# Optimization experiments

Hardware: AMD Instinct MI355X
Metric: run time of the kernel (lower is better)

The kernel has to match this reference:

```python
import jax, jax.numpy as jnp
import numpy as np

B, S, D, H = 2, 2048, 1024, 16
HD = D // H  # head_dim = 64

def setup_inputs() -> dict:
    key = jax.random.key(0)
    ks = jax.random.split(key, 6)
    scale = 1.0 / np.sqrt(D)  # ~xavier for square matrices
    return {
        "x": jax.random.normal(ks[0], (B, S, D), dtype=jnp.float32),
        "Wq": jax.random.normal(ks[1], (D, D), dtype=jnp.float32) * scale,
        "bq": jnp.zeros((D,), dtype=jnp.float32),
        "Wk": jax.random.normal(ks[2], (D, D), dtype=jnp.float32) * scale,
        "bk": jnp.zeros((D,), dtype=jnp.float32),
        "Wv": jax.random.normal(ks[3], (D, D), dtype=jnp.float32) * scale,
        "bv": jnp.zeros((D,), dtype=jnp.float32),
        "Wo": jax.random.normal(ks[4], (D, D), dtype=jnp.float32) * scale,
        "bo": jnp.zeros((D,), dtype=jnp.float32),
    }

def reference(x, Wq, bq, Wk, bk, Wv, bv, Wo, bo):
    b, s, d = x.shape
    # projections (torch Linear: x @ W^T + b)
    q = (x @ Wq.T + bq).reshape(b, s, H, HD).transpose(0, 2, 1, 3)  # [b,h,s,hd]
    k = (x @ Wk.T + bk).reshape(b, s, H, HD).transpose(0, 2, 1, 3)
    v = (x @ Wv.T + bv).reshape(b, s, H, HD).transpose(0, 2, 1, 3)
    scores = jnp.einsum('bhqd,bhkd->bhqk', q, k) / jnp.sqrt(jnp.float32(HD))
    attn = jax.nn.softmax(scores, axis=-1)  # dropout is identity in eval mode
    out = jnp.einsum('bhqk,bhkd->bhqd', attn, v)
    out = out.transpose(0, 2, 1, 3).reshape(b, s, d)
    return out @ Wo.T + bo
```

## Files before the change

kernel.cpp:

```cpp
#include <hip/hip_runtime.h>
#include <hip/hip_bf16.h>

constexpr int NH   = 16;
constexpr int SEQ  = 2048;
constexpr int DM   = 1024;
constexpr int HDIM = 64;

typedef __attribute__((ext_vector_type(4)))  float f32x4;
typedef __attribute__((ext_vector_type(16))) float f32x16;
typedef __attribute__((ext_vector_type(8)))  short bf16x8;

typedef __attribute__((address_space(3))) unsigned int lds_u32_t;
typedef const __attribute__((address_space(1))) unsigned int glb_u32_t;

__device__ __forceinline__ void gll16(const void* g, void* l) {
  __builtin_amdgcn_global_load_lds((glb_u32_t*)g, (lds_u32_t*)l, 16, 0, 0);
}

__device__ __forceinline__ ushort f2bf(float f) {
  union { float f; unsigned u; } v; v.f = f;
  unsigned u = v.u;
  return (ushort)((u + 0x7fffu + ((u >> 16) & 1u)) >> 16);
}

__device__ __forceinline__ float fast_exp2(float x) {
#if __has_builtin(__builtin_amdgcn_exp2f)
  return __builtin_amdgcn_exp2f(x);
#else
  return __expf(x * 0.69314718056f);
#endif
}

__device__ __forceinline__ unsigned cvtpk(float a, float b) {
  unsigned r;
  asm("v_cvt_pk_bf16_f32 %0, %1, %2" : "=v"(r) : "v"(a), "v"(b));
  return r;
}

__device__ __forceinline__ void plswap(unsigned &a, unsigned &b) {
  asm("v_permlane32_swap_b32 %0, %1" : "+v"(a), "+v"(b));
}

__global__ void cast_all(const float* __restrict__ x,
                         const float* __restrict__ wq, const float* __restrict__ wk,
                         const float* __restrict__ wv, const float* __restrict__ wo,
                         ushort* __restrict__ xb, ushort* __restrict__ wqkv,
                         ushort* __restrict__ wob) {
  const int i = blockIdx.x * blockDim.x + threadIdx.x;
  const float* src; ushort* dst; int off;
  if (i < 1048576)      { src = x;  dst = xb;             off = i; }
  else if (i < 1310720) { src = wq; dst = wqkv;           off = i - 1048576; }
  else if (i < 1572864) { src = wk; dst = wqkv + 1048576; off = i - 1310720; }
  else if (i < 1835008) { src = wv; dst = wqkv + 2097152; off = i - 1572864; }
  else                  { src = wo; dst = wob;            off = i - 1835008; }
  const float4 v = reinterpret_cast<const float4*>(src)[off];
  ushort4 o;
  o.x = f2bf(v.x); o.y = f2bf(v.y); o.z = f2bf(v.z); o.w = f2bf(v.w);
  reinterpret_cast<ushort4*>(dst)[off] = o;
}

__global__ __launch_bounds__(256) void gemm_qkv(
    const ushort* __restrict__ A, const ushort* __restrict__ Bw,
    const float* __restrict__ bq, const float* __restrict__ bk, const float* __restrict__ bv,
    ushort* __restrict__ qh, ushort* __restrict__ kh, ushort* __restrict__ vth)
{
  __shared__ ushort As[128 * 32];
  __shared__ ushort Bs[128 * 32];
  const int tid = threadIdx.x;
  const int lane = tid & 63, wid = tid >> 6;
  const int wr = wid >> 1, wc = wid & 1;
  const int l15 = lane & 15, lhi = lane >> 4;
  const int bm = blockIdx.x, bn = blockIdx.y;

  f32x4 acc[4][4] = {};

  const int strow = tid >> 2;
  const int stcol = (tid & 3) * 8;
  const ushort* Ag0 = A  + (size_t)(bm * 128 + strow) * 1024 + stcol;
  const ushort* Ag1 = Ag0 + 64 * 1024;
  const ushort* Bg0 = Bw + (size_t)(bn * 128 + strow) * 1024 + stcol;
  const ushort* Bg1 = Bg0 + 64 * 1024;
  ushort* Asl = As + tid * 8;
  ushort* Bsl = Bs + tid * 8;

  for (int k0 = 0; k0 < 1024; k0 += 32) {
    gll16(Ag0 + k0, Asl);
    gll16(Ag1 + k0, Asl + 2048);
    gll16(Bg0 + k0, Bsl);
    gll16(Bg1 + k0, Bsl + 2048);
    __syncthreads();
    bf16x8 af[4], bf[4];
#pragma unroll
    for (int i = 0; i < 4; i++)
      af[i] = *reinterpret_cast<const bf16x8*>(As + (wr * 64 + i * 16 + l15) * 32 + lhi * 8);
#pragma unroll
    for (int j = 0; j < 4; j++)
      bf[j] = *reinterpret_cast<const bf16x8*>(Bs + (wc * 64 + j * 16 + l15) * 32 + lhi * 8);
#pragma unroll
    for (int i = 0; i < 4; i++)
#pragma unroll
      for (int j = 0; j < 4; j++)
        acc[i][j] = __builtin_amdgcn_mfma_f32_16x16x32_bf16(af[i], bf[j], acc[i][j], 0, 0, 0);
    __syncthreads();
  }

  const int ncol0 = bn * 128 + wc * 64;
  const int mrow0 = bm * 128 + wr * 64;
  const int which = ncol0 >> 10;

  if (which == 2) {
#pragma unroll
    for (int i = 0; i < 4; i++) {
#pragma unroll
      for (int j = 0; j < 4; j++) {
        const int nn = (ncol0 + j * 16 + l15) & 1023;
        const int h = nn >> 6, hd = nn & 63;
        const float bias = bv[nn];
        const int m0 = mrow0 + i * 16 + lhi * 4;
        const int b = m0 >> 11, s = m0 & 2047;
        ushort4 pk;
        pk.x = f2bf(acc[i][j][0] + bias);
        pk.y = f2bf(acc[i][j][1] + bias);
        pk.z = f2bf(acc[i][j][2] + bias);
        pk.w = f2bf(acc[i][j][3] + bias);
        *reinterpret_cast<ushort4*>(
            &vth[((size_t)(b * NH + h) * HDIM + hd) * SEQ + s]) = pk;
      }
    }
  } else {
    const float scl = (which == 0) ? 0.18033688f : 1.0f;
    const float* __restrict__ bptr = (which == 0) ? bq : bk;
    ushort* __restrict__ dst = (which == 0) ? qh : kh;
#pragma unroll
    for (int i = 0; i < 4; i++) {
#pragma unroll
      for (int j = 0; j < 4; j++) {
        const int nn = (ncol0 + j * 16 + l15) & 1023;
        const int h = nn >> 6, hd = nn & 63;
        const float bias = bptr[nn];
#pragma unroll
        for (int jr = 0; jr < 4; jr++) {
          const int m = mrow0 + i * 16 + lhi * 4 + jr;
          const int b = m >> 11, s = m & 2047;
          dst[((size_t)(b * NH + h) * SEQ + s) * HDIM + hd] = f2bf((acc[i][j][jr] + bias) * scl);
        }
      }
    }
  }
}

__global__ __launch_bounds__(512, 2) void attn_kernel(
    const ushort* __restrict__ qh, const ushort* __restrict__ kh,
    const ushort* __restrict__ vth, ushort* __restrict__ ctx)
{
  __shared__ __align__(16) ushort Kt[2][64 * 64];
  __shared__ __align__(16) ushort Vt[2][64 * 64];
  __shared__ float linv_s[8][32];
  const int tid = threadIdx.x, lane = tid & 63, wid = tid >> 6;
  const int l31 = lane & 31, hi = lane >> 5;
  const int bh = blockIdx.y;
  const int q0 = blockIdx.x * 256;
  const int qw = q0 + wid * 32;
  const int rswz = (lane & 7) << 4;
  const int hi16 = hi * 16;

  bf16x8 qf[4];
  const ushort* qb = qh + (size_t)bh * SEQ * HDIM;
#pragma unroll
  for (int st = 0; st < 4; st++)
    qf[st] = *reinterpret_cast<const bf16x8*>(
        qb + (size_t)(qw + l31) * HDIM + st * 16 + hi * 8);

  f32x16 o0 = {}, o1 = {};
  float mrow = -INFINITY, lrow = 0.f;

  const int srow = tid >> 3;
  const int scole = (((tid & 7) * 16) ^ ((srow & 7) << 4)) >> 1;
  const ushort* kbase = kh + (size_t)bh * SEQ * HDIM;
  const ushort* vbase = vth + (size_t)bh * HDIM * SEQ;

  auto stage = [&](int buf, int kv0) {
    gll16(kbase + (size_t)(kv0 + srow) * HDIM + scole, &Kt[buf][tid * 8]);
    gll16(vbase + (size_t)srow * SEQ + kv0 + scole, &Vt[buf][tid * 8]);
  };

  stage(0, 0);
  __syncthreads();

  for (int t = 0; t < SEQ / 64; ++t) {
    const int cur = t & 1;
    if (t < SEQ / 64 - 1) stage(cur ^ 1, (t + 1) * 64);

    const char* kb = (const char*)Kt[cur];
    bf16x8 kf0[4], kf1[4];
#pragma unroll
    for (int st = 0; st < 4; st++) {
      kf0[st] = *reinterpret_cast<const bf16x8*>(kb + l31 * 128 + ((st * 32 + hi16) ^ rswz));
      kf1[st] = *reinterpret_cast<const bf16x8*>(kb + (32 + l31) * 128 + ((st * 32 + hi16) ^ rswz));
    }
    f32x16 acc0 = {}, acc1 = {};
    __builtin_amdgcn_s_setprio(1);
#pragma unroll
    for (int st = 0; st < 4; st++) {
      acc0 = __builtin_amdgcn_mfma_f32_32x32x16_bf16(kf0[st], qf[st], acc0, 0, 0, 0);
      acc1 = __builtin_amdgcn_mfma_f32_32x32x16_bf16(kf1[st], qf[st], acc1, 0, 0, 0);
    }
    __builtin_amdgcn_s_setprio(0);

    float tm[8];
#pragma unroll
    for (int r = 0; r < 8; r++)
      tm[r] = fmaxf(fmaxf(acc0[r], acc0[r + 8]), fmaxf(acc1[r], acc1[r + 8]));
    float mx = fmaxf(fmaxf(fmaxf(tm[0], tm[1]), fmaxf(tm[2], tm[3])),
                     fmaxf(fmaxf(tm[4], tm[5]), fmaxf(tm[6], tm[7])));
    mx = fmaxf(mx, __shfl_xor(mx, 32));
    if (__any(mx > mrow + 8.0f)) {
      const float mnew = fmaxf(mrow, mx);
      const float alpha = fast_exp2(mrow - mnew);
      mrow = mnew;
      lrow *= alpha;
      o0 *= alpha; o1 *= alpha;
    }
    float p0[16], p1[16];
#pragma unroll
    for (int r = 0; r < 16; r++) {
      p0[r] = fast_exp2(acc0[r] - mrow);
      p1[r] = fast_exp2(acc1[r] - mrow);
    }
    float ss[8];
#pragma unroll
    for (int r = 0; r < 8; r++) ss[r] = (p0[r] + p0[r + 8]) + (p1[r] + p1[r + 8]);
    float rs = ((ss[0] + ss[1]) + (ss[2] + ss[3])) + ((ss[4] + ss[5]) + (ss[6] + ss[7]));
    rs += __shfl_xor(rs, 32);
    lrow += rs;

    union PU { unsigned u[4]; bf16x8 v; };
    PU pa[4];
    {
      unsigned a0 = cvtpk(p0[0], p0[1]),   b0 = cvtpk(p0[4], p0[5]);   plswap(a0, b0);
      unsigned a1 = cvtpk(p0[2], p0[3]),   b1 = cvtpk(p0[6], p0[7]);   plswap(a1, b1);
      unsigned a2 = cvtpk(p0[8], p0[9]),   b2 = cvtpk(p0[12], p0[13]); plswap(a2, b2);
      unsigned a3 = cvtpk(p0[10], p0[11]), b3 = cvtpk(p0[14], p0[15]); plswap(a3, b3);
      pa[0].u[0] = a0; pa[0].u[1] = a1; pa[0].u[2] = b0; pa[0].u[3] = b1;
      pa[1].u[0] = a2; pa[1].u[1] = a3; pa[1].u[2] = b2; pa[1].u[3] = b3;
      unsigned c0 = cvtpk(p1[0], p1[1]),   d0 = cvtpk(p1[4], p1[5]);   plswap(c0, d0);
      unsigned c1 = cvtpk(p1[2], p1[3]),   d1 = cvtpk(p1[6], p1[7]);   plswap(c1, d1);
      unsigned c2 = cvtpk(p1[8], p1[9]),   d2 = cvtpk(p1[12], p1[13]); plswap(c2, d2);
      unsigned c3 = cvtpk(p1[10], p1[11]), d3 = cvtpk(p1[14], p1[15]); plswap(c3, d3);
      pa[2].u[0] = c0; pa[2].u[1] = c1; pa[2].u[2] = d0; pa[2].u[3] = d1;
      pa[3].u[0] = c2; pa[3].u[1] = c3; pa[3].u[2] = d2; pa[3].u[3] = d3;
    }

    const char* vb = (const char*)Vt[cur];
    bf16x8 bv0[4], bv1[4];
#pragma unroll
    for (int st = 0; st < 4; st++) {
      bv0[st] = *reinterpret_cast<const bf16x8*>(vb + l31 * 128 + ((st * 32 + hi16) ^ rswz));
      bv1[st] = *reinterpret_cast<const bf16x8*>(vb + (32 + l31) * 128 + ((st * 32 + hi16) ^ rswz));
    }
    __builtin_amdgcn_s_setprio(1);
#pragma unroll
    for (int st = 0; st < 4; st++) {
      o0 = __builtin_amdgcn_mfma_f32_32x32x16_bf16(pa[st].v, bv0[st], o0, 0, 0, 0);
      o1 = __builtin_amdgcn_mfma_f32_32x32x16_bf16(pa[st].v, bv1[st], o1, 0, 0, 0);
    }
    __builtin_amdgcn_s_setprio(0);

    __syncthreads();
  }

  const int b = bh >> 4, h = bh & 15;
  linv_s[wid][l31] = 1.0f / lrow;
  ushort* cb = ctx + (size_t)b * SEQ * DM + (size_t)h * HDIM;
#pragma unroll
  for (int r = 0; r < 16; r++) {
    const int qrow = (r & 3) + 8 * (r >> 2) + 4 * hi;
    const float iv = linv_s[wid][qrow];
    ushort* rp = cb + (size_t)(qw + qrow) * DM;
    rp[l31]      = f2bf(o0[r] * iv);
    rp[32 + l31] = f2bf(o1[r] * iv);
  }
}

__global__ __launch_bounds__(256) void gemm_out(
    const ushort* __restrict__ A, const ushort* __restrict__ Bw,
    const float* __restrict__ bo, float* __restrict__ out)
{
  __shared__ ushort As[128 * 32];
  __shared__ ushort Bs[128 * 32];
  const int tid = threadIdx.x;
  const int lane = tid & 63, wid = tid >> 6;
  const int wr = wid >> 1, wc = wid & 1;
  const int l15 = lane & 15, lhi = lane >> 4;
  const int bm = blockIdx.x, bn = blockIdx.y;

  f32x4 acc[4][4] = {};

  const int strow = tid >> 2;
  const int stcol = (tid & 3) * 8;
  const ushort* Ag0 = A  + (size_t)(bm * 128 + strow) * 1024 + stcol;
  const ushort* Ag1 = Ag0 + 64 * 1024;
  const ushort* Bg0 = Bw + (size_t)(bn * 128 + strow) * 1024 + stcol;
  const ushort* Bg1 = Bg0 + 64 * 1024;
  ushort* Asl = As + tid * 8;
  ushort* Bsl = Bs + tid * 8;

  for (int k0 = 0; k0 < 1024; k0 += 32) {
    gll16(Ag0 + k0, Asl);
    gll16(Ag1 + k0, Asl + 2048);
    gll16(Bg0 + k0, Bsl);
    gll16(Bg1 + k0, Bsl + 2048);
    __syncthreads();
    bf16x8 af[4], bf[4];
#pragma unroll
    for (int i = 0; i < 4; i++)
      af[i] = *reinterpret_cast<const bf16x8*>(As + (wr * 64 + i * 16 + l15) * 32 + lhi * 8);
#pragma unroll
    for (int j = 0; j < 4; j++)
      bf[j] = *reinterpret_cast<const bf16x8*>(Bs + (wc * 64 + j * 16 + l15) * 32 + lhi * 8);
#pragma unroll
    for (int i = 0; i < 4; i++)
#pragma unroll
      for (int j = 0; j < 4; j++)
        acc[i][j] = __builtin_amdgcn_mfma_f32_16x16x32_bf16(af[i], bf[j], acc[i][j], 0, 0, 0);
    __syncthreads();
  }

  const int ncol0 = bn * 128 + wc * 64;
  const int mrow0 = bm * 128 + wr * 64;
#pragma unroll
  for (int i = 0; i < 4; i++)
#pragma unroll
    for (int j = 0; j < 4; j++) {
      const int n = ncol0 + j * 16 + l15;
      const float bias = bo[n];
#pragma unroll
      for (int jr = 0; jr < 4; jr++) {
        const int m = mrow0 + i * 16 + lhi * 4 + jr;
        out[(size_t)m * 1024 + n] = acc[i][j][jr] + bias;
      }
    }
}

extern "C" void kernel_launch(void* const* d_in, const int* in_sizes, int n_in,
                              void* d_out, int out_size, void* d_ws, size_t ws_size,
                              hipStream_t stream) {
  (void)in_sizes; (void)n_in; (void)out_size; (void)ws_size;
  const float* x  = (const float*)d_in[0];
  const float* Wq = (const float*)d_in[1];
  const float* bq = (const float*)d_in[2];
  const float* Wk = (const float*)d_in[3];
  const float* bk = (const float*)d_in[4];
  const float* Wv = (const float*)d_in[5];
  const float* bv = (const float*)d_in[6];
  const float* Wo = (const float*)d_in[7];
  const float* bo = (const float*)d_in[8];
  float* out = (float*)d_out;

  char* ws = (char*)d_ws;
  ushort* xb   = (ushort*)(ws);
  ushort* wqkv = (ushort*)(ws + 8388608);
  ushort* wob  = (ushort*)(ws + 14680064);
  ushort* qhb  = (ushort*)(ws + 16777216);
  ushort* khb  = (ushort*)(ws + 25165824);
  ushort* vth  = (ushort*)(ws + 33554432);
  ushort* ctx  = (ushort*)(ws + 41943040);

  cast_all<<<8192, 256, 0, stream>>>(x, Wq, Wk, Wv, Wo, xb, wqkv, wob);
  gemm_qkv<<<dim3(32, 24), 256, 0, stream>>>(xb, wqkv, bq, bk, bv, qhb, khb, vth);
  attn_kernel<<<dim3(8, 32), 512, 0, stream>>>(qhb, khb, vth, ctx);
  gemm_out<<<dim3(32, 8), 256, 0, stream>>>(ctx, wob, bo, out);
}
```

Before: 214.4 us.

## Double-buffer GEMM tiles, enlarge attention KV tile to 128, remap attention grid

Both projection GEMMs now keep two LDS buffers and issue the global-to-LDS loads for the next K slice before computing the current one, with one barrier per step instead of two. The attention kernel now processes 128 keys per iteration instead of 64, with new swizzles for the wider V tile and K fragments loaded in chunks. It also uses a 1D grid where consecutive blocks walk the heads first. This halves the attention loop's barriers and per-tile softmax overhead, and aims to overlap GEMM loads with MFMA work, at the cost of doubled LDS use and higher register pressure in attention, which could reduce occupancy.

```diff
diff --git a/kernel.cpp b/kernel.cpp
--- a/kernel.cpp
+++ b/kernel.cpp
@@ -64,8 +64,8 @@
     const float* __restrict__ bq, const float* __restrict__ bk, const float* __restrict__ bv,
     ushort* __restrict__ qh, ushort* __restrict__ kh, ushort* __restrict__ vth)
 {
-  __shared__ ushort As[128 * 32];
-  __shared__ ushort Bs[128 * 32];
+  __shared__ ushort As[2][128 * 32];
+  __shared__ ushort Bs[2][128 * 32];
   const int tid = threadIdx.x;
   const int lane = tid & 63, wid = tid >> 6;
   const int wr = wid >> 1, wc = wid & 1;
@@ -80,22 +80,27 @@
   const ushort* Ag1 = Ag0 + 64 * 1024;
   const ushort* Bg0 = Bw + (size_t)(bn * 128 + strow) * 1024 + stcol;
   const ushort* Bg1 = Bg0 + 64 * 1024;
-  ushort* Asl = As + tid * 8;
-  ushort* Bsl = Bs + tid * 8;
-
-  for (int k0 = 0; k0 < 1024; k0 += 32) {
-    gll16(Ag0 + k0, Asl);
-    gll16(Ag1 + k0, Asl + 2048);
-    gll16(Bg0 + k0, Bsl);
-    gll16(Bg1 + k0, Bsl + 2048);
-    __syncthreads();
+
+  auto stage = [&](int buf, int k0) {
+    gll16(Ag0 + k0, &As[buf][tid * 8]);
+    gll16(Ag1 + k0, &As[buf][tid * 8 + 2048]);
+    gll16(Bg0 + k0, &Bs[buf][tid * 8]);
+    gll16(Bg1 + k0, &Bs[buf][tid * 8 + 2048]);
+  };
+
+  stage(0, 0);
+  __syncthreads();
+
+  for (int kk = 0; kk < 32; ++kk) {
+    const int cur = kk & 1;
+    if (kk < 31) stage(cur ^ 1, (kk + 1) * 32);
     bf16x8 af[4], bf[4];
 #pragma unroll
     for (int i = 0; i < 4; i++)
-      af[i] = *reinterpret_cast<const bf16x8*>(As + (wr * 64 + i * 16 + l15) * 32 + lhi * 8);
+      af[i] = *reinterpret_cast<const bf16x8*>(&As[cur][(wr * 64 + i * 16 + l15) * 32 + lhi * 8]);
 #pragma unroll
     for (int j = 0; j < 4; j++)
-      bf[j] = *reinterpret_cast<const bf16x8*>(Bs + (wc * 64 + j * 16 + l15) * 32 + lhi * 8);
+      bf[j] = *reinterpret_cast<const bf16x8*>(&Bs[cur][(wc * 64 + j * 16 + l15) * 32 + lhi * 8]);
 #pragma unroll
     for (int i = 0; i < 4; i++)
 #pragma unroll
@@ -153,15 +158,17 @@
     const ushort* __restrict__ qh, const ushort* __restrict__ kh,
     const ushort* __restrict__ vth, ushort* __restrict__ ctx)
 {
-  __shared__ __align__(16) ushort Kt[2][64 * 64];
-  __shared__ __align__(16) ushort Vt[2][64 * 64];
+  __shared__ __align__(16) ushort Kt[2][128 * 64];
+  __shared__ __align__(16) ushort Vt[2][64 * 128];
   __shared__ float linv_s[8][32];
   const int tid = threadIdx.x, lane = tid & 63, wid = tid >> 6;
   const int l31 = lane & 31, hi = lane >> 5;
-  const int bh = blockIdx.y;
-  const int q0 = blockIdx.x * 256;
+  const int bid = blockIdx.x;
+  const int bh = bid & 31;
+  const int q0 = (bid >> 5) * 256;
   const int qw = q0 + wid * 32;
-  const int rswz = (lane & 7) << 4;
+  const int kswz = (l31 & 7) << 4;
+  const int vswz = (l31 & 15) << 4;
   const int hi16 = hi * 16;
 
   bf16x8 qf[4];
@@ -174,45 +181,78 @@
   f32x16 o0 = {}, o1 = {};
   float mrow = -INFINITY, lrow = 0.f;
 
-  const int srow = tid >> 3;
-  const int scole = (((tid & 7) * 16) ^ ((srow & 7) << 4)) >> 1;
+  const int srK = tid >> 3;
+  const int scK = (((tid & 7) * 16) ^ ((srK & 7) << 4)) >> 1;
+  const int srV = tid >> 4;
+  const int scV = (((tid & 15) * 16) ^ ((srV & 15) << 4)) >> 1;
   const ushort* kbase = kh + (size_t)bh * SEQ * HDIM;
   const ushort* vbase = vth + (size_t)bh * HDIM * SEQ;
 
   auto stage = [&](int buf, int kv0) {
-    gll16(kbase + (size_t)(kv0 + srow) * HDIM + scole, &Kt[buf][tid * 8]);
-    gll16(vbase + (size_t)srow * SEQ + kv0 + scole, &Vt[buf][tid * 8]);
+    gll16(kbase + (size_t)(kv0 + srK) * HDIM + scK,      &Kt[buf][tid * 8]);
+    gll16(kbase + (size_t)(kv0 + 64 + srK) * HDIM + scK, &Kt[buf][tid * 8 + 4096]);
+    gll16(vbase + (size_t)srV * SEQ + kv0 + scV,         &Vt[buf][tid * 8]);
+    gll16(vbase + (size_t)(32 + srV) * SEQ + kv0 + scV,  &Vt[buf][tid * 8 + 4096]);
   };
 
   stage(0, 0);
   __syncthreads();
 
-  for (int t = 0; t < SEQ / 64; ++t) {
+  union PU { unsigned u[4]; bf16x8 v; };
+  auto mkpa = [&](const f32x16& p, PU& lo, PU& hi_) {
+    unsigned a0 = cvtpk(p[0], p[1]),   b0 = cvtpk(p[4], p[5]);   plswap(a0, b0);
+    unsigned a1 = cvtpk(p[2], p[3]),   b1 = cvtpk(p[6], p[7]);   plswap(a1, b1);
+    unsigned a2 = cvtpk(p[8], p[9]),   b2 = cvtpk(p[12], p[13]); plswap(a2, b2);
+    unsigned a3 = cvtpk(p[10], p[11]), b3 = cvtpk(p[14], p[15]); plswap(a3, b3);
+    lo.u[0] = a0;  lo.u[1] = a1;  lo.u[2] = b0;  lo.u[3] = b1;
+    hi_.u[0] = a2; hi_.u[1] = a3; hi_.u[2] = b2; hi_.u[3] = b3;
+  };
+
+  for (int t = 0; t < SEQ / 128; ++t) {
     const int cur = t & 1;
-    if (t < SEQ / 64 - 1) stage(cur ^ 1, (t + 1) * 64);
+    if (t < SEQ / 128 - 1) stage(cur ^ 1, (t + 1) * 128);
 
     const char* kb = (const char*)Kt[cur];
-    bf16x8 kf0[4], kf1[4];
-#pragma unroll
-    for (int st = 0; st < 4; st++) {
-      kf0[st] = *reinterpret_cast<const bf16x8*>(kb + l31 * 128 + ((st * 32 + hi16) ^ rswz));
-      kf1[st] = *reinterpret_cast<const bf16x8*>(kb + (32 + l31) * 128 + ((st * 32 + hi16) ^ rswz));
-    }
-    f32x16 acc0 = {}, acc1 = {};
+    f32x16 acc0 = {}, acc1 = {}, acc2 = {}, acc3 = {};
     __builtin_amdgcn_s_setprio(1);
-#pragma unroll
-    for (int st = 0; st < 4; st++) {
-      acc0 = __builtin_amdgcn_mfma_f32_32x32x16_bf16(kf0[st], qf[st], acc0, 0, 0, 0);
-      acc1 = __builtin_amdgcn_mfma_f32_32x32x16_bf16(kf1[st], qf[st], acc1, 0, 0, 0);
+    {
+      bf16x8 kf[4];
+#pragma unroll
+      for (int st = 0; st < 4; st++)
+        kf[st] = *reinterpret_cast<const bf16x8*>(kb + l31 * 128 + ((st * 32 + hi16) ^ kswz));
+#pragma unroll
+      for (int st = 0; st < 4; st++)
+        acc0 = __builtin_amdgcn_mfma_f32_32x32x16_bf16(kf[st], qf[st], acc0, 0, 0, 0);
+#pragma unroll
+      for (int st = 0; st < 4; st++)
+        kf[st] = *reinterpret_cast<const bf16x8*>(kb + (32 + l31) * 128 + ((st * 32 + hi16) ^ kswz));
+#pragma unroll
+      for (int st = 0; st < 4; st++)
+        acc1 = __builtin_amdgcn_mfma_f32_32x32x16_bf16(kf[st], qf[st], acc1, 0, 0, 0);
+#pragma unroll
+      for (int st = 0; st < 4; st++)
+        kf[st] = *reinterpret_cast<const bf16x8*>(kb + (64 + l31) * 128 + ((st * 32 + hi16) ^ kswz));
+#pragma unroll
+      for (int st = 0; st < 4; st++)
+        acc2 = __builtin_amdgcn_mfma_f32_32x32x16_bf16(kf[st], qf[st], acc2, 0, 0, 0);
+#pragma unroll
+      for (int st = 0; st < 4; st++)
+        kf[st] = *reinterpret_cast<const bf16x8*>(kb + (96 + l31) * 128 + ((st * 32 + hi16) ^ kswz));
+#pragma unroll
+      for (int st = 0; st < 4; st++)
+        acc3 = __builtin_amdgcn_mfma_f32_32x32x16_bf16(kf[st], qf[st], acc3, 0, 0, 0);
     }
     __builtin_amdgcn_s_setprio(0);
 
-    float tm[8];
-#pragma unroll
-    for (int r = 0; r < 8; r++)
-      tm[r] = fmaxf(fmaxf(acc0[r], acc0[r + 8]), fmaxf(acc1[r], acc1[r + 8]));
-    float mx = fmaxf(fmaxf(fmaxf(tm[0], tm[1]), fmaxf(tm[2], tm[3])),
-                     fmaxf(fmaxf(tm[4], tm[5]), fmaxf(tm[6], tm[7])));
+    float tm[16];
+#pragma unroll
+    for (int r = 0; r < 16; r++)
+      tm[r] = fmaxf(fmaxf(acc0[r], acc1[r]), fmaxf(acc2[r], acc3[r]));
+#pragma unroll
+    for (int d = 8; d >= 1; d >>= 1)
+#pragma unroll
+      for (int r = 0; r < d; r++) tm[r] = fmaxf(tm[r], tm[r + d]);
+    float mx = tm[0];
     mx = fmaxf(mx, __shfl_xor(mx, 32));
     if (__any(mx > mrow + 8.0f)) {
       const float mnew = fmaxf(mrow, mx);
@@ -221,48 +261,39 @@
       lrow *= alpha;
       o0 *= alpha; o1 *= alpha;
     }
-    float p0[16], p1[16];
+    f32x16 pb0, pb1, pb2, pb3;
 #pragma unroll
     for (int r = 0; r < 16; r++) {
-      p0[r] = fast_exp2(acc0[r] - mrow);
-      p1[r] = fast_exp2(acc1[r] - mrow);
-    }
-    float ss[8];
-#pragma unroll
-    for (int r = 0; r < 8; r++) ss[r] = (p0[r] + p0[r + 8]) + (p1[r] + p1[r + 8]);
-    float rs = ((ss[0] + ss[1]) + (ss[2] + ss[3])) + ((ss[4] + ss[5]) + (ss[6] + ss[7]));
+      pb0[r] = fast_exp2(acc0[r] - mrow);
+      pb1[r] = fast_exp2(acc1[r] - mrow);
+      pb2[r] = fast_exp2(acc2[r] - mrow);
+      pb3[r] = fast_exp2(acc3[r] - mrow);
+    }
+    float ss[16];
+#pragma unroll
+    for (int r = 0; r < 16; r++) ss[r] = (pb0[r] + pb1[r]) + (pb2[r] + pb3[r]);
+#pragma unroll
+    for (int d = 8; d >= 1; d >>= 1)
+#pragma unroll
+      for (int r = 0; r < d; r++) ss[r] += ss[r + d];
+    float rs = ss[0];
     rs += __shfl_xor(rs, 32);
     lrow += rs;
 
-    union PU { unsigned u[4]; bf16x8 v; };
-    PU pa[4];
-    {
-      unsigned a0 = cvtpk(p0[0], p0[1]),   b0 = cvtpk(p0[4], p0[5]);   plswap(a0, b0);
-      unsigned a1 = cvtpk(p0[2], p0[3]),   b1 = cvtpk(p0[6], p0[7]);   plswap(a1, b1);
-      unsigned a2 = cvtpk(p0[8], p0[9]),   b2 = cvtpk(p0[12], p0[13]); plswap(a2, b2);
-      unsigned a3 = cvtpk(p0[10], p0[11]), b3 = cvtpk(p0[14], p0[15]); plswap(a3, b3);
-      pa[0].u[0] = a0; pa[0].u[1] = a1; pa[0].u[2] = b0; pa[0].u[3] = b1;
-      pa[1].u[0] = a2; pa[1].u[1] = a3; pa[1].u[2] = b2; pa[1].u[3] = b3;
-      unsigned c0 = cvtpk(p1[0], p1[1]),   d0 = cvtpk(p1[4], p1[5]);   plswap(c0, d0);
-      unsigned c1 = cvtpk(p1[2], p1[3]),   d1 = cvtpk(p1[6], p1[7]);   plswap(c1, d1);
-      unsigned c2 = cvtpk(p1[8], p1[9]),   d2 = cvtpk(p1[12], p1[13]); plswap(c2, d2);
-      unsigned c3 = cvtpk(p1[10], p1[11]), d3 = cvtpk(p1[14], p1[15]); plswap(c3, d3);
-      pa[2].u[0] = c0; pa[2].u[1] = c1; pa[2].u[2] = d0; pa[2].u[3] = d1;
-      pa[3].u[0] = c2; pa[3].u[1] = c3; pa[3].u[2] = d2; pa[3].u[3] = d3;
-    }
+    PU pa[8];
+    mkpa(pb0, pa[0], pa[1]);
+    mkpa(pb1, pa[2], pa[3]);
+    mkpa(pb2, pa[4], pa[5]);
+    mkpa(pb3, pa[6], pa[7]);
 
     const char* vb = (const char*)Vt[cur];
-    bf16x8 bv0[4], bv1[4];
-#pragma unroll
-    for (int st = 0; st < 4; st++) {
-      bv0[st] = *reinterpret_cast<const bf16x8*>(vb + l31 * 128 + ((st * 32 + hi16) ^ rswz));
-      bv1[st] = *reinterpret_cast<const bf16x8*>(vb + (32 + l31) * 128 + ((st * 32 + hi16) ^ rswz));
-    }
     __builtin_amdgcn_s_setprio(1);
 #pragma unroll
-    for (int st = 0; st < 4; st++) {
-      o0 = __builtin_amdgcn_mfma_f32_32x32x16_bf16(pa[st].v, bv0[st], o0, 0, 0, 0);
-      o1 = __builtin_amdgcn_mfma_f32_32x32x16_bf16(pa[st].v, bv1[st], o1, 0, 0, 0);
+    for (int st = 0; st < 8; st++) {
+      const bf16x8 b0 = *reinterpret_cast<const bf16x8*>(vb + l31 * 256 + ((st * 32 + hi16) ^ vswz));
+      const bf16x8 b1 = *reinterpret_cast<const bf16x8*>(vb + (32 + l31) * 256 + ((st * 32 + hi16) ^ vswz));
+      o0 = __builtin_amdgcn_mfma_f32_32x32x16_bf16(pa[st].v, b0, o0, 0, 0, 0);
+      o1 = __builtin_amdgcn_mfma_f32_32x32x16_bf16(pa[st].v, b1, o1, 0, 0, 0);
     }
     __builtin_amdgcn_s_setprio(0);
 
@@ -286,8 +317,8 @@
     const ushort* __restrict__ A, const ushort* __restrict__ Bw,
     const float* __restrict__ bo, float* __restrict__ out)
 {
-  __shared__ ushort As[128 * 32];
-  __shared__ ushort Bs[128 * 32];
+  __shared__ ushort As[2][128 * 32];
+  __shared__ ushort Bs[2][128 * 32];
   const int tid = threadIdx.x;
   const int lane = tid & 63, wid = tid >> 6;
   const int wr = wid >> 1, wc = wid & 1;
@@ -302,22 +333,27 @@
   const ushort* Ag1 = Ag0 + 64 * 1024;
   const ushort* Bg0 = Bw + (size_t)(bn * 128 + strow) * 1024 + stcol;
   const ushort* Bg1 = Bg0 + 64 * 1024;
-  ushort* Asl = As + tid * 8;
-  ushort* Bsl = Bs + tid * 8;
-
-  for (int k0 = 0; k0 < 1024; k0 += 32) {
-    gll16(Ag0 + k0, Asl);
-    gll16(Ag1 + k0, Asl + 2048);
-    gll16(Bg0 + k0, Bsl);
-    gll16(Bg1 + k0, Bsl + 2048);
-    __syncthreads();
+
+  auto stage = [&](int buf, int k0) {
+    gll16(Ag0 + k0, &As[buf][tid * 8]);
+    gll16(Ag1 + k0, &As[buf][tid * 8 + 2048]);
+    gll16(Bg0 + k0, &Bs[buf][tid * 8]);
+    gll16(Bg1 + k0, &Bs[buf][tid * 8 + 2048]);
+  };
+
+  stage(0, 0);
+  __syncthreads();
+
+  for (int kk = 0; kk < 32; ++kk) {
+    const int cur = kk & 1;
+    if (kk < 31) stage(cur ^ 1, (kk + 1) * 32);
     bf16x8 af[4], bf[4];
 #pragma unroll
     for (int i = 0; i < 4; i++)
-      af[i] = *reinterpret_cast<const bf16x8*>(As + (wr * 64 + i * 16 + l15) * 32 + lhi * 8);
+      af[i] = *reinterpret_cast<const bf16x8*>(&As[cur][(wr * 64 + i * 16 + l15) * 32 + lhi * 8]);
 #pragma unroll
     for (int j = 0; j < 4; j++)
-      bf[j] = *reinterpret_cast<const bf16x8*>(Bs + (wc * 64 + j * 16 + l15) * 32 + lhi * 8);
+      bf[j] = *reinterpret_cast<const bf16x8*>(&Bs[cur][(wc * 64 + j * 16 + l15) * 32 + lhi * 8]);
 #pragma unroll
     for (int i = 0; i < 4; i++)
 #pragma unroll
@@ -368,6 +404,6 @@
 
   cast_all<<<8192, 256, 0, stream>>>(x, Wq, Wk, Wv, Wo, xb, wqkv, wob);
   gemm_qkv<<<dim3(32, 24), 256, 0, stream>>>(xb, wqkv, bq, bk, bv, qhb, khb, vth);
-  attn_kernel<<<dim3(8, 32), 512, 0, stream>>>(qhb, khb, vth, ctx);
+  attn_kernel<<<256, 512, 0, stream>>>(qhb, khb, vth, ctx);
   gemm_out<<<dim3(32, 8), 256, 0, stream>>>(ctx, wob, bo, out);
 }
```

Result: no change. 215.7 us (+0.6%).
